# Kernel optimization log

Hardware: AMD Instinct MI355X
Metric: run time of the kernel (lower is better)

Reference implementation:

```python
import jax, jax.numpy as jnp
import numpy as np
from jax import lax

C = 256
HEADS = 8
H2 = HEADS // 2          # heads per branch
HD = C // HEADS          # head dim = 32
SR = 4                   # spatial reduction ratio
WS = 7                   # window size (hard-coded in source)
SCALE = HD ** -0.5
EPS = 1e-5


def _window_partition(t, H, W, D):
    # t: [B, h, N, c] -> [B*h*nW, WS^3, c]
    B, h, N, c = t.shape
    t = t.reshape(B * h, H // WS, WS, W // WS, WS, D // WS, WS, c)
    t = t.transpose(0, 1, 3, 5, 2, 4, 6, 7)
    return t.reshape(-1, WS * WS * WS, c)


def _window_reverse(w, H, W, D, head):
    # w: [BH*nW, WS^3, c] -> [B, N, head*c] (heads interleaved into channels)
    nW = (H // WS) * (W // WS) * (D // WS)
    BH = w.shape[0] // nW
    x = w.reshape(BH, H // WS, W // WS, D // WS, WS, WS, WS, -1)
    x = x.transpose(0, 1, 4, 2, 5, 3, 6, 7).reshape(BH, H, W, D, -1)
    B = BH // head
    x = x.reshape(B, head, H, W, D, -1).transpose(0, 2, 3, 4, 1, 5)
    return x.reshape(B, H * W * D, -1)


def setup_inputs() -> dict:
    key = jax.random.key(0)
    ks = jax.random.split(key, 16)
    B, H, W, D = 1, 28, 28, 28
    N = H * W * D
    tn = lambda k, shp: jax.random.normal(k, shp, jnp.float32) * 0.02
    # conv fan-out inits (per source _init_weights)
    lepe_fan = 3 * 3 * C // C  # depthwise: groups=C
    sr_fan = SR * SR * C
    return {
        "x": jax.random.normal(ks[0], (B, N, C), jnp.float32),
        "H": H, "W": W, "D": D,
        "lepe_w": tn(ks[1], (C, C)),
        "lepe_b": jnp.zeros((C,), jnp.float32),
        "lepe_conv_w": jax.random.normal(ks[2], (C, 1, 3, 3, 3), jnp.float32) * np.sqrt(2.0 / lepe_fan),
        "lepe_conv_b": jnp.zeros((C,), jnp.float32),
        "sr_w": jax.random.normal(ks[3], (C, C, SR, SR, SR), jnp.float32) * np.sqrt(2.0 / sr_fan),
        "sr_b": jnp.zeros((C,), jnp.float32),
        "norm_g": jnp.ones((C,), jnp.float32),
        "norm_b": jnp.zeros((C,), jnp.float32),
        "q1_w": tn(ks[4], (C // 2, C)),
        "kv1_w": tn(ks[5], (C, C)),
        "q2_w": tn(ks[6], (C // 2, C)),
        "kv2_w": tn(ks[7], (C, C)),
        "proj_w": tn(ks[8], (C, C)),
        "proj_b": jnp.zeros((C,), jnp.float32),
    }


def _forward(x, lepe_w, lepe_b, lepe_conv_w, lepe_conv_b, sr_w, sr_b,
             norm_g, norm_b, q1_w, kv1_w, q2_w, kv2_w, proj_w, proj_b,
             H, W, D):
    B, N, _ = x.shape
    # --- LePE: linear -> depthwise Conv3d over (H,W,D) ---
    y = x @ lepe_w.T + lepe_b                              # [B,N,C]
    y = y.transpose(0, 2, 1).reshape(B, C, H, W, D)
    lepe = lax.conv_general_dilated(
        y, lepe_conv_w, window_strides=(1, 1, 1), padding='SAME',
        dimension_numbers=('NCDHW', 'OIDHW', 'NCDHW'), feature_group_count=C)
    lepe = (lepe + lepe_conv_b[None, :, None, None, None])
    lepe = lepe.reshape(B, C, N).transpose(0, 2, 1)        # [B,N,C]

    x_ = x.transpose(0, 2, 1).reshape(B, C, H, W, D)

    # --- Branch 1: spatially-reduced global attention (heads 0..3) ---
    q1 = (x @ q1_w.T).reshape(B, N, H2, HD).transpose(0, 2, 1, 3)   # [B,h2,N,hd]
    x1 = lax.conv_general_dilated(
        x_, sr_w, window_strides=(SR, SR, SR), padding='VALID',
        dimension_numbers=('NCDHW', 'OIDHW', 'NCDHW'))
    x1 = x1 + sr_b[None, :, None, None, None]
    x1 = x1.reshape(B, C, -1).transpose(0, 2, 1)                    # [B,Nr,C]
    mu = x1.mean(-1, keepdims=True)
    var = ((x1 - mu) ** 2).mean(-1, keepdims=True)
    x1 = (x1 - mu) * lax.rsqrt(var + EPS) * norm_g + norm_b
    x1 = jax.nn.gelu(x1, approximate=False)
    Nr = x1.shape[1]
    kv1 = (x1 @ kv1_w.T).reshape(B, Nr, 2, H2, HD).transpose(2, 0, 3, 1, 4)
    k1, v1 = kv1[0], kv1[1]                                         # [B,h2,Nr,hd]
    attn1 = jax.nn.softmax(jnp.einsum('bhnd,bhmd->bhnm', q1, k1) * SCALE, axis=-1)
    o1 = jnp.einsum('bhnm,bhmd->bhnd', attn1, v1)
    o1 = o1.transpose(0, 2, 1, 3).reshape(B, N, C // 2)

    # --- Branch 2: windowed local attention (heads 4..7) ---
    q2 = (x @ q2_w.T).reshape(B, N, H2, HD).transpose(0, 2, 1, 3)
    kv2 = (x @ kv2_w.T).reshape(B, N, 2, H2, HD).transpose(2, 0, 3, 1, 4)
    k2, v2 = kv2[0], kv2[1]                                         # [B,h2,N,hd]
    q2w = _window_partition(q2, H, W, D)
    k2w = _window_partition(k2, H, W, D)
    v2w = _window_partition(v2, H, W, D)
    attn2 = jax.nn.softmax(jnp.einsum('wnd,wmd->wnm', q2w, k2w) * SCALE, axis=-1)
    o2 = jnp.einsum('wnm,wmd->wnd', attn2, v2w)
    o2 = _window_reverse(o2, H, W, D, H2)                           # [B,N,C/2]

    out = jnp.concatenate([o1, o2], axis=-1)
    return (out + lepe) @ proj_w.T + proj_b


def reference(x, H, W, D, lepe_w, lepe_b, lepe_conv_w, lepe_conv_b,
              sr_w, sr_b, norm_g, norm_b, q1_w, kv1_w, q2_w, kv2_w,
              proj_w, proj_b):
    return _forward(x, lepe_w, lepe_b, lepe_conv_w, lepe_conv_b, sr_w, sr_b,
                    norm_g, norm_b, q1_w, kv1_w, q2_w, kv2_w, proj_w, proj_b,
                    int(H), int(W), int(D))
```

## Files before the change

### kernel.cpp

```cpp
#include <hip/hip_runtime.h>

#define N_TOK 21952
#define NR    343
#define ATT_SCALE 0.17677669529663687f

typedef unsigned short u16;
typedef short  v8s __attribute__((ext_vector_type(8)));
typedef float  v4f __attribute__((ext_vector_type(4)));

__device__ __forceinline__ float bf2f(unsigned u) {
    return __builtin_bit_cast(float, u << 16);
}
__device__ __forceinline__ u16 f2bf(float f) {
    unsigned u = __builtin_bit_cast(unsigned, f);
    u += 0x7fffu + ((u >> 16) & 1u);
    return (u16)(u >> 16);
}
__device__ __forceinline__ unsigned bfadd2(unsigned a, unsigned b) {
    float lo = bf2f(a & 0xffffu) + bf2f(b & 0xffffu);
    float hi = bf2f(a >> 16)     + bf2f(b >> 16);
    return (unsigned)f2bf(lo) | ((unsigned)f2bf(hi) << 16);
}

__global__ __launch_bounds__(256) void convert_x_kernel(
    const float* __restrict__ x, u16* __restrict__ xb)
{
    size_t i = ((size_t)blockIdx.x * 256 + threadIdx.x) * 8;
    float4 a0 = *(const float4*)(x + i);
    float4 a1 = *(const float4*)(x + i + 4);
    uint4 av;
    av.x = (unsigned)f2bf(a0.x) | ((unsigned)f2bf(a0.y) << 16);
    av.y = (unsigned)f2bf(a0.z) | ((unsigned)f2bf(a0.w) << 16);
    av.z = (unsigned)f2bf(a1.x) | ((unsigned)f2bf(a1.y) << 16);
    av.w = (unsigned)f2bf(a1.z) | ((unsigned)f2bf(a1.w) << 16);
    *(uint4*)(xb + i) = av;
}

#define WSEG0 16384
#define WSEG1 24576
#define WSEG2 32768
#define WSEG3 49152
#define WSEG4 65536
#define WSEG5 81920
#define WSEG6 82112

__global__ __launch_bounds__(256) void convert_w_kernel(
    const float* __restrict__ wl,  const float* __restrict__ wq1,
    const float* __restrict__ wq2, const float* __restrict__ wk2,
    const float* __restrict__ wk1, const float* __restrict__ wp,
    const float* __restrict__ lepe_b,
    u16* wb_comb, u16* wb_k1, u16* wb_p, float* bias_all)
{
    int gid = blockIdx.x * 256 + threadIdx.x;
    if (gid >= WSEG6) return;
    if (gid >= WSEG5) {
        int b = gid - WSEG5;
        float4 v;
        int i = b * 4;
        v.x = (i + 0 < 256) ? lepe_b[i + 0] : 0.f;
        v.y = (i + 1 < 256) ? lepe_b[i + 1] : 0.f;
        v.z = (i + 2 < 256) ? lepe_b[i + 2] : 0.f;
        v.w = (i + 3 < 256) ? lepe_b[i + 3] : 0.f;
        *(float4*)(bias_all + i) = v;
        return;
    }
    const float* s; u16* d; int l; float sc = 1.f;
    if      (gid < WSEG0) { s = wl;  d = wb_comb;           l = gid; }
    else if (gid < WSEG1) { s = wq1; d = wb_comb + 65536;   l = gid - WSEG0; sc = ATT_SCALE; }
    else if (gid < WSEG2) { s = wq2; d = wb_comb + 98304;   l = gid - WSEG1; sc = ATT_SCALE; }
    else if (gid < WSEG3) { s = wk2; d = wb_comb + 131072;  l = gid - WSEG2; }
    else if (gid < WSEG4) { s = wk1; d = wb_k1;             l = gid - WSEG3; }
    else                  { s = wp;  d = wb_p;              l = gid - WSEG4; }
    float4 v = *(const float4*)(s + (size_t)l * 4);
    *(ushort4*)(d + (size_t)l * 4) =
        make_ushort4(f2bf(v.x * sc), f2bf(v.y * sc), f2bf(v.z * sc), f2bf(v.w * sc));
}

__global__ __launch_bounds__(256) void convert_sr_kernel(
    const float* __restrict__ wsr, u16* __restrict__ wt)
{
    int u  = blockIdx.x * 256 + threadIdx.x;
    int co = u >> 8, ci = u & 255;
    const float* src = wsr + (size_t)co * 16384 + ci * 64;
#pragma unroll
    for (int t4 = 0; t4 < 16; t4++) {
        float4 v = *(const float4*)(src + t4 * 4);
        int t = t4 * 4;
        wt[(size_t)(t + 0) * 65536 + co * 256 + ci] = f2bf(v.x);
        wt[(size_t)(t + 1) * 65536 + co * 256 + ci] = f2bf(v.y);
        wt[(size_t)(t + 2) * 65536 + co * 256 + ci] = f2bf(v.z);
        wt[(size_t)(t + 3) * 65536 + co * 256 + ci] = f2bf(v.w);
    }
}

#define LDA 40

__global__ __launch_bounds__(256) void gemm_bf16(
    const void* __restrict__ A, const u16* __restrict__ A2,
    const u16* __restrict__ W, const float* __restrict__ bias,
    void* __restrict__ outp, int M, int K, int ldout, int a_fp32, int mode)
{
    __shared__ u16 Asm[128 * LDA];
    __shared__ u16 Bsm[128 * LDA];
    const int tid = threadIdx.x;
    const int m0 = blockIdx.x * 128;
    const int n0 = blockIdx.y * 128;
    const int wave = tid >> 6, lane = tid & 63;
    const int wm = (wave & 1) * 64, wn = (wave >> 1) * 64;
    const int fr = lane & 15, fq = lane >> 4;

    v4f acc[4][4];
#pragma unroll
    for (int i = 0; i < 4; i++)
#pragma unroll
        for (int j = 0; j < 4; j++) acc[i][j] = (v4f){0.f, 0.f, 0.f, 0.f};

    for (int kk = 0; kk < K; kk += 32) {
#pragma unroll
        for (int i = 0; i < 2; i++) {
            int u = tid + i * 256;
            int r = u >> 2, kc = (u & 3) * 8;
            uint4 av = make_uint4(0, 0, 0, 0);
            int m = m0 + r;
            if (m < M) {
                if (a_fp32) {
                    const float* Af = (const float*)A + (size_t)m * K + kk + kc;
                    float4 a0 = *(const float4*)Af;
                    float4 a1 = *(const float4*)(Af + 4);
                    av.x = (unsigned)f2bf(a0.x) | ((unsigned)f2bf(a0.y) << 16);
                    av.y = (unsigned)f2bf(a0.z) | ((unsigned)f2bf(a0.w) << 16);
                    av.z = (unsigned)f2bf(a1.x) | ((unsigned)f2bf(a1.y) << 16);
                    av.w = (unsigned)f2bf(a1.z) | ((unsigned)f2bf(a1.w) << 16);
                } else {
                    av = *(const uint4*)((const u16*)A + (size_t)m * K + kk + kc);
                    if (A2) {
                        uint4 bv = *(const uint4*)(A2 + (size_t)m * K + kk + kc);
                        av.x = bfadd2(av.x, bv.x); av.y = bfadd2(av.y, bv.y);
                        av.z = bfadd2(av.z, bv.z); av.w = bfadd2(av.w, bv.w);
                    }
                }
            }
            *(uint4*)(Asm + r * LDA + kc) = av;
            uint4 wv = *(const uint4*)(W + (size_t)(n0 + r) * K + kk + kc);
            *(uint4*)(Bsm + r * LDA + kc) = wv;
        }
        __syncthreads();

        v8s af[4], bfr[4];
#pragma unroll
        for (int i = 0; i < 4; i++)
            af[i] = *(const v8s*)(Asm + (wm + i * 16 + fr) * LDA + fq * 8);
#pragma unroll
        for (int j = 0; j < 4; j++)
            bfr[j] = *(const v8s*)(Bsm + (wn + j * 16 + fr) * LDA + fq * 8);
#pragma unroll
        for (int i = 0; i < 4; i++)
#pragma unroll
            for (int j = 0; j < 4; j++)
                acc[i][j] = __builtin_amdgcn_mfma_f32_16x16x32_bf16(
                    af[i], bfr[j], acc[i][j], 0, 0, 0);
        __syncthreads();
    }

    float* outf = (float*)outp;
    u16*   outb = (u16*)outp;
#pragma unroll
    for (int i = 0; i < 4; i++) {
#pragma unroll
        for (int j = 0; j < 4; j++) {
            int col = n0 + wn + j * 16 + fr;
#pragma unroll
            for (int r = 0; r < 4; r++) {
                int row = m0 + wm + i * 16 + fq * 4 + r;
                if (row >= M) continue;
                float v = acc[i][j][r];
                if (bias) v += bias[col];
                if (mode == 0) outb[(size_t)row * ldout + col] = f2bf(v);
                else           outf[(size_t)row * ldout + col] = v;
            }
        }
    }
}

__global__ __launch_bounds__(256) void sr_gemm(
    const u16* __restrict__ xb, const u16* __restrict__ Wt,
    float* __restrict__ partials)
{
    __shared__ u16 Asm[128 * LDA];
    __shared__ u16 Bsm[128 * LDA];
    const int tid = threadIdx.x;
    const int m0 = blockIdx.x * 128;
    const int n0 = blockIdx.y * 128;
    const int z  = blockIdx.z;
    const int wave = tid >> 6, lane = tid & 63;
    const int wm = (wave & 1) * 64, wn = (wave >> 1) * 64;
    const int fr = lane & 15, fq = lane >> 4;

    v4f acc[4][4];
#pragma unroll
    for (int i = 0; i < 4; i++)
#pragma unroll
        for (int j = 0; j < 4; j++) acc[i][j] = (v4f){0.f, 0.f, 0.f, 0.f};

    for (int it = 0; it < 16; it++) {
        int tap = z * 2 + (it >> 3);
        int ci0 = (it & 7) * 32;
        int kz = tap >> 4, ky = (tap >> 2) & 3, kx = tap & 3;
#pragma unroll
        for (int i = 0; i < 2; i++) {
            int u = tid + i * 256;
            int r = u >> 2, seg = (u & 3) * 8;
            uint4 av = make_uint4(0, 0, 0, 0);
            int p = m0 + r;
            if (p < NR) {
                int pz = p / 49, pr = p % 49, py = pr / 7, px = pr % 7;
                int n = (pz * 4 + kz) * 784 + (py * 4 + ky) * 28 + (px * 4 + kx);
                av = *(const uint4*)(xb + (size_t)n * 256 + ci0 + seg);
            }
            *(uint4*)(Asm + r * LDA + seg) = av;
            uint4 wv = *(const uint4*)(Wt + (size_t)tap * 65536 +
                                       (size_t)(n0 + r) * 256 + ci0 + seg);
            *(uint4*)(Bsm + r * LDA + seg) = wv;
        }
        __syncthreads();

        v8s af[4], bfr[4];
#pragma unroll
        for (int i = 0; i < 4; i++)
            af[i] = *(const v8s*)(Asm + (wm + i * 16 + fr) * LDA + fq * 8);
#pragma unroll
        for (int j = 0; j < 4; j++)
            bfr[j] = *(const v8s*)(Bsm + (wn + j * 16 + fr) * LDA + fq * 8);
#pragma unroll
        for (int i = 0; i < 4; i++)
#pragma unroll
            for (int j = 0; j < 4; j++)
                acc[i][j] = __builtin_amdgcn_mfma_f32_16x16x32_bf16(
                    af[i], bfr[j], acc[i][j], 0, 0, 0);
        __syncthreads();
    }

    float* dst = partials + (size_t)z * (NR * 256);
#pragma unroll
    for (int i = 0; i < 4; i++) {
#pragma unroll
        for (int j = 0; j < 4; j++) {
            int col = n0 + wn + j * 16 + fr;
#pragma unroll
            for (int r = 0; r < 4; r++) {
                int row = m0 + wm + i * 16 + fq * 4 + r;
                if (row < NR) dst[(size_t)row * 256 + col] = acc[i][j][r];
            }
        }
    }
}

__global__ __launch_bounds__(256) void ln_gelu_kernel(
    const float* __restrict__ partials, const float* __restrict__ srb,
    const float* __restrict__ g, const float* __restrict__ b,
    u16* __restrict__ out)
{
    int row = blockIdx.x, c = threadIdx.x;
    float v = srb[c];
#pragma unroll
    for (int s = 0; s < 32; s++)
        v += partials[(size_t)s * (NR * 256) + row * 256 + c];
    float s1 = v, s2 = v * v;
#pragma unroll
    for (int off = 1; off < 64; off <<= 1) {
        s1 += __shfl_xor(s1, off);
        s2 += __shfl_xor(s2, off);
    }
    __shared__ float ws[4], ws2[4];
    int wave = c >> 6, lane = c & 63;
    if (lane == 0) { ws[wave] = s1; ws2[wave] = s2; }
    __syncthreads();
    float mean = (ws[0] + ws[1] + ws[2] + ws[3]) * (1.f / 256.f);
    float m2   = (ws2[0] + ws2[1] + ws2[2] + ws2[3]) * (1.f / 256.f);
    float var  = m2 - mean * mean;
    float xn = (v - mean) * rsqrtf(var + 1e-5f) * g[c] + b[c];
    out[row * 256 + c] = f2bf(0.5f * xn * (1.f + erff(xn * 0.70710678118654752f)));
}

__global__ __launch_bounds__(256) void dwconv_kernel(
    const u16* __restrict__ xall, const float* __restrict__ w,
    const float* __restrict__ bias, u16* __restrict__ out)
{
    __shared__ float sm[216 * 64];
    __shared__ float sw[64 * 27];
    const int tid = threadIdx.x;
    const int t  = blockIdx.x;
    const int g  = blockIdx.y;
    const int tz = t / 49, tr = t % 49, ty = tr / 7, tx = tr % 7;

    for (int u = tid; u < 64 * 27; u += 256) sw[u] = w[g * 64 * 27 + u];

    for (int u = tid; u < 216 * 8; u += 256) {
        int r = u >> 3, c8 = (u & 7) * 8;
        int vz = tz * 4 - 1 + r / 36;
        int rem = r % 36;
        int vy = ty * 4 - 1 + rem / 6;
        int vx = tx * 4 - 1 + rem % 6;
        float f[8];
        if ((unsigned)vz < 28u && (unsigned)vy < 28u && (unsigned)vx < 28u) {
            int n = vz * 784 + vy * 28 + vx;
            uint4 raw = *(const uint4*)(xall + (size_t)n * 768 + g * 64 + c8);
            f[0] = bf2f(raw.x & 0xffffu); f[1] = bf2f(raw.x >> 16);
            f[2] = bf2f(raw.y & 0xffffu); f[3] = bf2f(raw.y >> 16);
            f[4] = bf2f(raw.z & 0xffffu); f[5] = bf2f(raw.z >> 16);
            f[6] = bf2f(raw.w & 0xffffu); f[7] = bf2f(raw.w >> 16);
        } else {
#pragma unroll
            for (int i = 0; i < 8; i++) f[i] = 0.f;
        }
        float* dst = &sm[r * 64 + c8];
        *(float4*)dst       = make_float4(f[0], f[1], f[2], f[3]);
        *(float4*)(dst + 4) = make_float4(f[4], f[5], f[6], f[7]);
    }
    __syncthreads();

    const int c  = tid & 63;
    const int ch = g * 64 + c;
    float wreg[27];
#pragma unroll
    for (int j = 0; j < 27; j++) wreg[j] = sw[c * 27 + j];
    const float bc = bias[ch];

    const int vbase = (tid >> 6) * 16;
    for (int v = vbase; v < vbase + 16; v++) {
        int vz = v >> 4, vy = (v >> 2) & 3, vx = v & 3;
        float a = bc;
#pragma unroll
        for (int dz = 0; dz < 3; dz++)
#pragma unroll
            for (int dy = 0; dy < 3; dy++)
#pragma unroll
                for (int dx = 0; dx < 3; dx++)
                    a = fmaf(sm[((vz + dz) * 36 + (vy + dy) * 6 + (vx + dx)) * 64 + c],
                             wreg[dz * 9 + dy * 3 + dx], a);
        int n = (tz * 4 + vz) * 784 + (ty * 4 + vy) * 28 + (tx * 4 + vx);
        out[(size_t)n * 256 + ch] = f2bf(a);
    }
}

#define KP  40
#define VTP 360
#define PP  40

__global__ __launch_bounds__(256) void attn1_kernel(
    const u16* __restrict__ xall, const u16* __restrict__ kv1,
    u16* __restrict__ o)
{
    __shared__ u16 Ks[352 * KP];
    __shared__ u16 VTs[32 * VTP];
    __shared__ u16 Ps[4 * 16 * PP];
    const int tid = threadIdx.x;
    const int h = blockIdx.y;
    const int qbase = blockIdx.x * 352;
    const int mt0 = blockIdx.z * 11;
    const int wave = tid >> 6, lane = tid & 63;
    const int fr = lane & 15, fq = lane >> 4;

    for (int u = tid; u < 352 * 4; u += 256) {
        int r = u >> 2, seg = u & 3;
        uint4 kq = make_uint4(0, 0, 0, 0), vq = make_uint4(0, 0, 0, 0);
        if (r < NR) {
            kq = *(const uint4*)(kv1 + (size_t)r * 256 + h * 32 + seg * 8);
            vq = *(const uint4*)(kv1 + (size_t)r * 256 + 128 + h * 32 + seg * 8);
        }
        *(uint4*)(Ks + r * KP + seg * 8) = kq;
        int d0 = seg * 8;
        VTs[(d0 + 0) * VTP + r] = (u16)(vq.x & 0xffffu);
        VTs[(d0 + 1) * VTP + r] = (u16)(vq.x >> 16);
        VTs[(d0 + 2) * VTP + r] = (u16)(vq.y & 0xffffu);
        VTs[(d0 + 3) * VTP + r] = (u16)(vq.y >> 16);
        VTs[(d0 + 4) * VTP + r] = (u16)(vq.z & 0xffffu);
        VTs[(d0 + 5) * VTP + r] = (u16)(vq.z >> 16);
        VTs[(d0 + 6) * VTP + r] = (u16)(vq.w & 0xffffu);
        VTs[(d0 + 7) * VTP + r] = (u16)(vq.w >> 16);
    }
    __syncthreads();

    u16* Pw = Ps + wave * 16 * PP;
    for (int mt = mt0 + wave; mt < mt0 + 11; mt += 4) {
        int qrow = qbase + mt * 16 + fr;
        v8s aq = {0, 0, 0, 0, 0, 0, 0, 0};
        if (qrow < N_TOK)
            aq = *(const v8s*)(xall + (size_t)qrow * 768 + 256 + h * 32 + fq * 8);

        v4f s[22];
#pragma unroll
        for (int t = 0; t < 22; t++) {
            v8s bk = *(const v8s*)(Ks + (t * 16 + fr) * KP + fq * 8);
            s[t] = __builtin_amdgcn_mfma_f32_16x16x32_bf16(
                aq, bk, (v4f){0.f, 0.f, 0.f, 0.f}, 0, 0, 0);
        }
        if (fr >= 7) {
#pragma unroll
            for (int r = 0; r < 4; r++) s[21][r] = -1e30f;
        }

        float inv_l[4];
#pragma unroll
        for (int r = 0; r < 4; r++) {
            float m = s[0][r];
#pragma unroll
            for (int t = 1; t < 22; t++) m = fmaxf(m, s[t][r]);
#pragma unroll
            for (int off = 1; off < 16; off <<= 1) m = fmaxf(m, __shfl_xor(m, off));
            float l = 0.f;
#pragma unroll
            for (int t = 0; t < 22; t++) {
                v4f sv = s[t];
                float p = __expf(sv[r] - m);
                sv[r] = p; s[t] = sv;
                l += p;
            }
#pragma unroll
            for (int off = 1; off < 16; off <<= 1) l += __shfl_xor(l, off);
            inv_l[r] = 1.f / l;
        }

        v4f o0 = {0.f, 0.f, 0.f, 0.f}, o1 = {0.f, 0.f, 0.f, 0.f};
#pragma unroll
        for (int kt = 0; kt < 11; kt++) {
#pragma unroll
            for (int tt = 0; tt < 2; tt++) {
                int t = kt * 2 + tt;
#pragma unroll
                for (int r = 0; r < 4; r++)
                    Pw[(fq * 4 + r) * PP + tt * 16 + fr] = f2bf(s[t][r]);
            }
            __asm__ volatile("s_waitcnt lgkmcnt(0)" ::: "memory");
            v8s ap  = *(const v8s*)(Pw + fr * PP + fq * 8);
            v8s bv0 = *(const v8s*)(VTs + fr * VTP + kt * 32 + fq * 8);
            v8s bv1 = *(const v8s*)(VTs + (16 + fr) * VTP + kt * 32 + fq * 8);
            o0 = __builtin_amdgcn_mfma_f32_16x16x32_bf16(ap, bv0, o0, 0, 0, 0);
            o1 = __builtin_amdgcn_mfma_f32_16x16x32_bf16(ap, bv1, o1, 0, 0, 0);
        }

#pragma unroll
        for (int r = 0; r < 4; r++) {
            int n = qbase + mt * 16 + fq * 4 + r;
            if (n < N_TOK) {
                u16* op = o + (size_t)n * 256 + h * 32;
                op[fr]      = f2bf(o0[r] * inv_l[r]);
                op[16 + fr] = f2bf(o1[r] * inv_l[r]);
            }
        }
    }
}

__global__ __launch_bounds__(256) void attn2_kernel(
    const u16* __restrict__ xall, u16* __restrict__ o)
{
    __shared__ u16 Ks[352 * KP];
    __shared__ u16 VTs[32 * VTP];
    __shared__ u16 Ps[4 * 16 * PP];
    const int tid = threadIdx.x;
    const int h  = blockIdx.y;
    const int wi = blockIdx.x;
    const int zb = (wi >> 4) & 3, yb = (wi >> 2) & 3, xb = wi & 3;
    const int mt0 = blockIdx.z * 11;
    const int wave = tid >> 6, lane = tid & 63;
    const int fr = lane & 15, fq = lane >> 4;

    for (int u = tid; u < 352 * 4; u += 256) {
        int r = u >> 2, seg = u & 3;
        uint4 kq = make_uint4(0, 0, 0, 0), vq = make_uint4(0, 0, 0, 0);
        if (r < NR) {
            int mz = r / 49, mr = r % 49, my = mr / 7, mx = mr % 7;
            int nk = (zb * 7 + mz) * 784 + (yb * 7 + my) * 28 + (xb * 7 + mx);
            const u16* base = xall + (size_t)nk * 768 + 512;
            kq = *(const uint4*)(base + h * 32 + seg * 8);
            vq = *(const uint4*)(base + 128 + h * 32 + seg * 8);
        }
        *(uint4*)(Ks + r * KP + seg * 8) = kq;
        int d0 = seg * 8;
        VTs[(d0 + 0) * VTP + r] = (u16)(vq.x & 0xffffu);
        VTs[(d0 + 1) * VTP + r] = (u16)(vq.x >> 16);
        VTs[(d0 + 2) * VTP + r] = (u16)(vq.y & 0xffffu);
        VTs[(d0 + 3) * VTP + r] = (u16)(vq.y >> 16);
        VTs[(d0 + 4) * VTP + r] = (u16)(vq.z & 0xffffu);
        VTs[(d0 + 5) * VTP + r] = (u16)(vq.z >> 16);
        VTs[(d0 + 6) * VTP + r] = (u16)(vq.w & 0xffffu);
        VTs[(d0 + 7) * VTP + r] = (u16)(vq.w >> 16);
    }
    __syncthreads();

    u16* Pw = Ps + wave * 16 * PP;
    for (int mt = mt0 + wave; mt < mt0 + 11; mt += 4) {
        int tw = mt * 16 + fr;
        v8s aq = {0, 0, 0, 0, 0, 0, 0, 0};
        if (tw < NR) {
            int wz = tw / 49, tr2 = tw % 49, wy = tr2 / 7, wx = tr2 % 7;
            int nq = (zb * 7 + wz) * 784 + (yb * 7 + wy) * 28 + (xb * 7 + wx);
            aq = *(const v8s*)(xall + (size_t)nq * 768 + 384 + h * 32 + fq * 8);
        }

        v4f s[22];
#pragma unroll
        for (int t = 0; t < 22; t++) {
            v8s bk = *(const v8s*)(Ks + (t * 16 + fr) * KP + fq * 8);
            s[t] = __builtin_amdgcn_mfma_f32_16x16x32_bf16(
                aq, bk, (v4f){0.f, 0.f, 0.f, 0.f}, 0, 0, 0);
        }
        if (fr >= 7) {
#pragma unroll
            for (int r = 0; r < 4; r++) s[21][r] = -1e30f;
        }

        float inv_l[4];
#pragma unroll
        for (int r = 0; r < 4; r++) {
            float m = s[0][r];
#pragma unroll
            for (int t = 1; t < 22; t++) m = fmaxf(m, s[t][r]);
#pragma unroll
            for (int off = 1; off < 16; off <<= 1) m = fmaxf(m, __shfl_xor(m, off));
            float l = 0.f;
#pragma unroll
            for (int t = 0; t < 22; t++) {
                v4f sv = s[t];
                float p = __expf(sv[r] - m);
                sv[r] = p; s[t] = sv;
                l += p;
            }
#pragma unroll
            for (int off = 1; off < 16; off <<= 1) l += __shfl_xor(l, off);
            inv_l[r] = 1.f / l;
        }

        v4f o0 = {0.f, 0.f, 0.f, 0.f}, o1 = {0.f, 0.f, 0.f, 0.f};
#pragma unroll
        for (int kt = 0; kt < 11; kt++) {
#pragma unroll
            for (int tt = 0; tt < 2; tt++) {
                int t = kt * 2 + tt;
#pragma unroll
                for (int r = 0; r < 4; r++)
                    Pw[(fq * 4 + r) * PP + tt * 16 + fr] = f2bf(s[t][r]);
            }
            __asm__ volatile("s_waitcnt lgkmcnt(0)" ::: "memory");
            v8s ap  = *(const v8s*)(Pw + fr * PP + fq * 8);
            v8s bv0 = *(const v8s*)(VTs + fr * VTP + kt * 32 + fq * 8);
            v8s bv1 = *(const v8s*)(VTs + (16 + fr) * VTP + kt * 32 + fq * 8);
            o0 = __builtin_amdgcn_mfma_f32_16x16x32_bf16(ap, bv0, o0, 0, 0, 0);
            o1 = __builtin_amdgcn_mfma_f32_16x16x32_bf16(ap, bv1, o1, 0, 0, 0);
        }

#pragma unroll
        for (int r = 0; r < 4; r++) {
            int ts = mt * 16 + fq * 4 + r;
            if (ts < NR) {
                int wz = ts / 49, tr2 = ts % 49, wy = tr2 / 7, wx = tr2 % 7;
                int nq = (zb * 7 + wz) * 784 + (yb * 7 + wy) * 28 + (xb * 7 + wx);
                u16* op = o + (size_t)nq * 256 + 128 + h * 32;
                op[fr]      = f2bf(o0[r] * inv_l[r]);
                op[16 + fr] = f2bf(o1[r] * inv_l[r]);
            }
        }
    }
}

extern "C" void kernel_launch(void* const* d_in, const int* in_sizes, int n_in,
                              void* d_out, int out_size, void* d_ws, size_t ws_size,
                              hipStream_t stream)
{
    const float* x       = (const float*)d_in[0];
    const float* lepe_w  = (const float*)d_in[4];
    const float* lepe_b  = (const float*)d_in[5];
    const float* lconv_w = (const float*)d_in[6];
    const float* lconv_b = (const float*)d_in[7];
    const float* sr_w    = (const float*)d_in[8];
    const float* sr_b    = (const float*)d_in[9];
    const float* norm_g  = (const float*)d_in[10];
    const float* norm_b  = (const float*)d_in[11];
    const float* q1_w    = (const float*)d_in[12];
    const float* kv1_w   = (const float*)d_in[13];
    const float* q2_w    = (const float*)d_in[14];
    const float* kv2_w   = (const float*)d_in[15];
    const float* proj_w  = (const float*)d_in[16];
    const float* proj_b  = (const float*)d_in[17];
    float* out = (float*)d_out;

    const size_t NC = (size_t)N_TOK * 256;

    float* partials = (float*)d_ws;
    float* bias_all = partials + 32 * (NR * 256);
    u16* xb     = (u16*)(bias_all + 768);
    u16* xall   = xb + NC;
    u16* lepeb  = xall + (size_t)N_TOK * 768;
    u16* colb   = lepeb + NC;
    u16* x1b    = colb + NC;
    u16* kv1b   = x1b + NR * 256;
    u16* wb_comb = kv1b + NR * 256;
    u16* wb_k1  = wb_comb + 196608;
    u16* wb_p   = wb_k1 + 65536;
    u16* wsr_t  = wb_p + 65536;
    size_t need = (size_t)(32 * NR * 256 + 768) * 4 +
                  (NC + (size_t)N_TOK * 768 + 3 * NC + 2 * (size_t)NR * 256 +
                   196608 + 2 * 65536 + 4194304) * 2;
    if (ws_size < need) return;

    convert_w_kernel<<<dim3(321), 256, 0, stream>>>(
        lepe_w, q1_w, q2_w, kv2_w, kv1_w, proj_w, lepe_b,
        wb_comb, wb_k1, wb_p, bias_all);
    convert_sr_kernel<<<dim3(256), 256, 0, stream>>>(sr_w, wsr_t);
    convert_x_kernel<<<dim3(2744), 256, 0, stream>>>(x, xb);
    gemm_bf16<<<dim3(172, 6), 256, 0, stream>>>(xb, nullptr, wb_comb, bias_all,
                                                xall, N_TOK, 256, 768, 0, 0);
    dwconv_kernel<<<dim3(343, 4), 256, 0, stream>>>(xall, lconv_w, lconv_b, lepeb);
    sr_gemm<<<dim3(3, 2, 32), 256, 0, stream>>>(xb, wsr_t, partials);
    ln_gelu_kernel<<<dim3(NR), 256, 0, stream>>>(partials, sr_b, norm_g, norm_b, x1b);
    gemm_bf16<<<dim3(3, 2), 256, 0, stream>>>(x1b, nullptr, wb_k1, nullptr,
                                              kv1b, NR, 256, 256, 0, 0);
    attn1_kernel<<<dim3(63, 4, 2), 256, 0, stream>>>(xall, kv1b, colb);
    attn2_kernel<<<dim3(64, 4, 2), 256, 0, stream>>>(xall, colb);
    gemm_bf16<<<dim3(172, 2), 256, 0, stream>>>(colb, lepeb, wb_p, proj_b,
                                                out, N_TOK, 256, 256, 0, 1);
}
```

Before: 293.4 us.

## Rewrite GEMMs as one-shot full-K 64x64 tiles with XOR-swizzled LDS

Replaces the K-looped 128x128 GEMM, which used a padded LDS tile and a barrier pair per K step, with a kernel that loads the whole K=256 slab of A and W into XOR-swizzled shared memory at once and then runs 8 MFMA steps without further barriers. Tiles shrink to 64x64, giving many more blocks, and the bf16 output is staged through LDS so global stores are coalesced 16-byte writes. The SR conv GEMM gets the same treatment, loading each tap's full channel range in one go. The cost is 64 KB of LDS per block, which limits occupancy, plus more redundant reloads of A and W from the smaller tiles.

```diff
diff --git a/kernel.cpp b/kernel.cpp
--- a/kernel.cpp
+++ b/kernel.cpp
@@ -21,6 +21,8 @@
     float hi = bf2f(a >> 16)     + bf2f(b >> 16);
     return (unsigned)f2bf(lo) | ((unsigned)f2bf(hi) << 16);
 }
+
+#define SWZ(r, g) ((((g) ^ ((r) & 7))) * 8)
 
 __global__ __launch_bounds__(256) void convert_x_kernel(
     const float* __restrict__ x, u16* __restrict__ xb)
@@ -93,158 +95,199 @@
     }
 }
 
-#define LDA 40
-
-__global__ __launch_bounds__(256) void gemm_bf16(
-    const void* __restrict__ A, const u16* __restrict__ A2,
+__global__ __launch_bounds__(256) void gemm_os(
+    const u16* __restrict__ A, const u16* __restrict__ A2,
     const u16* __restrict__ W, const float* __restrict__ bias,
-    void* __restrict__ outp, int M, int K, int ldout, int a_fp32, int mode)
-{
-    __shared__ u16 Asm[128 * LDA];
-    __shared__ u16 Bsm[128 * LDA];
+    void* __restrict__ outp, int M, int ldout, int mode)
+{
+    __shared__ u16 Asm[64 * 256];
+    __shared__ u16 Bsm[64 * 256];
     const int tid = threadIdx.x;
-    const int m0 = blockIdx.x * 128;
-    const int n0 = blockIdx.y * 128;
+    const int n0 = blockIdx.x * 64;
+    const int m0 = blockIdx.y * 64;
     const int wave = tid >> 6, lane = tid & 63;
-    const int wm = (wave & 1) * 64, wn = (wave >> 1) * 64;
+    const int wm = (wave & 1) * 32, wn = (wave >> 1) * 32;
     const int fr = lane & 15, fq = lane >> 4;
 
-    v4f acc[4][4];
-#pragma unroll
-    for (int i = 0; i < 4; i++)
-#pragma unroll
-        for (int j = 0; j < 4; j++) acc[i][j] = (v4f){0.f, 0.f, 0.f, 0.f};
-
-    for (int kk = 0; kk < K; kk += 32) {
+    uint4 pa[8], pb[8], pa2[8];
+#pragma unroll
+    for (int i = 0; i < 8; i++) {
+        int u = i * 256 + tid;
+        int r = u >> 5, seg = (u & 31) * 8;
+        int m = m0 + r;
+        uint4 av = make_uint4(0, 0, 0, 0);
+        if (m < M) av = *(const uint4*)(A + (size_t)m * 256 + seg);
+        pa[i] = av;
+        if (A2) {
+            uint4 bv = make_uint4(0, 0, 0, 0);
+            if (m < M) bv = *(const uint4*)(A2 + (size_t)m * 256 + seg);
+            pa2[i] = bv;
+        }
+        pb[i] = *(const uint4*)(W + (size_t)(n0 + r) * 256 + seg);
+    }
+#pragma unroll
+    for (int i = 0; i < 8; i++) {
+        int u = i * 256 + tid;
+        int r = u >> 5, g = u & 31;
+        uint4 av = pa[i];
+        if (A2) {
+            av.x = bfadd2(av.x, pa2[i].x); av.y = bfadd2(av.y, pa2[i].y);
+            av.z = bfadd2(av.z, pa2[i].z); av.w = bfadd2(av.w, pa2[i].w);
+        }
+        *(uint4*)(Asm + r * 256 + SWZ(r, g)) = av;
+        *(uint4*)(Bsm + r * 256 + SWZ(r, g)) = pb[i];
+    }
+    __syncthreads();
+
+    v4f acc[2][2];
+#pragma unroll
+    for (int i = 0; i < 2; i++)
+#pragma unroll
+        for (int j = 0; j < 2; j++) acc[i][j] = (v4f){0.f, 0.f, 0.f, 0.f};
+
+#pragma unroll
+    for (int ks = 0; ks < 8; ks++) {
+        v8s af[2], bfj[2];
 #pragma unroll
         for (int i = 0; i < 2; i++) {
-            int u = tid + i * 256;
-            int r = u >> 2, kc = (u & 3) * 8;
-            uint4 av = make_uint4(0, 0, 0, 0);
-            int m = m0 + r;
-            if (m < M) {
-                if (a_fp32) {
-                    const float* Af = (const float*)A + (size_t)m * K + kk + kc;
-                    float4 a0 = *(const float4*)Af;
-                    float4 a1 = *(const float4*)(Af + 4);
-                    av.x = (unsigned)f2bf(a0.x) | ((unsigned)f2bf(a0.y) << 16);
-                    av.y = (unsigned)f2bf(a0.z) | ((unsigned)f2bf(a0.w) << 16);
-                    av.z = (unsigned)f2bf(a1.x) | ((unsigned)f2bf(a1.y) << 16);
-                    av.w = (unsigned)f2bf(a1.z) | ((unsigned)f2bf(a1.w) << 16);
-                } else {
-                    av = *(const uint4*)((const u16*)A + (size_t)m * K + kk + kc);
-                    if (A2) {
-                        uint4 bv = *(const uint4*)(A2 + (size_t)m * K + kk + kc);
-                        av.x = bfadd2(av.x, bv.x); av.y = bfadd2(av.y, bv.y);
-                        av.z = bfadd2(av.z, bv.z); av.w = bfadd2(av.w, bv.w);
-                    }
+            int row = wm + i * 16 + fr;
+            af[i] = *(const v8s*)(Asm + row * 256 + SWZ(row, ks * 4 + fq));
+        }
+#pragma unroll
+        for (int j = 0; j < 2; j++) {
+            int row = wn + j * 16 + fr;
+            bfj[j] = *(const v8s*)(Bsm + row * 256 + SWZ(row, ks * 4 + fq));
+        }
+#pragma unroll
+        for (int i = 0; i < 2; i++)
+#pragma unroll
+            for (int j = 0; j < 2; j++)
+                acc[i][j] = __builtin_amdgcn_mfma_f32_16x16x32_bf16(
+                    af[i], bfj[j], acc[i][j], 0, 0, 0);
+    }
+
+    if (mode == 1) {
+        float* outf = (float*)outp;
+#pragma unroll
+        for (int i = 0; i < 2; i++)
+#pragma unroll
+            for (int j = 0; j < 2; j++) {
+                int col = n0 + wn + j * 16 + fr;
+                float bv = bias ? bias[col] : 0.f;
+#pragma unroll
+                for (int r = 0; r < 4; r++) {
+                    int row = m0 + wm + i * 16 + fq * 4 + r;
+                    if (row < M)
+                        outf[(size_t)row * ldout + col] = acc[i][j][r] + bv;
                 }
             }
-            *(uint4*)(Asm + r * LDA + kc) = av;
-            uint4 wv = *(const uint4*)(W + (size_t)(n0 + r) * K + kk + kc);
-            *(uint4*)(Bsm + r * LDA + kc) = wv;
-        }
-        __syncthreads();
-
-        v8s af[4], bfr[4];
-#pragma unroll
-        for (int i = 0; i < 4; i++)
-            af[i] = *(const v8s*)(Asm + (wm + i * 16 + fr) * LDA + fq * 8);
-#pragma unroll
-        for (int j = 0; j < 4; j++)
-            bfr[j] = *(const v8s*)(Bsm + (wn + j * 16 + fr) * LDA + fq * 8);
-#pragma unroll
-        for (int i = 0; i < 4; i++)
-#pragma unroll
-            for (int j = 0; j < 4; j++)
-                acc[i][j] = __builtin_amdgcn_mfma_f32_16x16x32_bf16(
-                    af[i], bfr[j], acc[i][j], 0, 0, 0);
-        __syncthreads();
-    }
-
-    float* outf = (float*)outp;
-    u16*   outb = (u16*)outp;
-#pragma unroll
-    for (int i = 0; i < 4; i++) {
-#pragma unroll
-        for (int j = 0; j < 4; j++) {
-            int col = n0 + wn + j * 16 + fr;
+        return;
+    }
+    __syncthreads();
+    u16* ot = Asm;
+#pragma unroll
+    for (int i = 0; i < 2; i++)
+#pragma unroll
+        for (int j = 0; j < 2; j++) {
+            int col = wn + j * 16 + fr;
+            float bv = bias ? bias[n0 + col] : 0.f;
 #pragma unroll
             for (int r = 0; r < 4; r++) {
-                int row = m0 + wm + i * 16 + fq * 4 + r;
-                if (row >= M) continue;
-                float v = acc[i][j][r];
-                if (bias) v += bias[col];
-                if (mode == 0) outb[(size_t)row * ldout + col] = f2bf(v);
-                else           outf[(size_t)row * ldout + col] = v;
-            }
-        }
-    }
-}
-
-__global__ __launch_bounds__(256) void sr_gemm(
+                int row = wm + i * 16 + fq * 4 + r;
+                ot[row * 72 + col] = f2bf(acc[i][j][r] + bv);
+            }
+        }
+    __syncthreads();
+    u16* outb = (u16*)outp;
+#pragma unroll
+    for (int k2 = 0; k2 < 2; k2++) {
+        int u = k2 * 256 + tid;
+        int r = u >> 3, cs = (u & 7) * 8;
+        int row = m0 + r;
+        if (row < M)
+            *(uint4*)(outb + (size_t)row * ldout + n0 + cs) =
+                *(const uint4*)(ot + r * 72 + cs);
+    }
+}
+
+__global__ __launch_bounds__(256) void sr_gemm_os(
     const u16* __restrict__ xb, const u16* __restrict__ Wt,
     float* __restrict__ partials)
 {
-    __shared__ u16 Asm[128 * LDA];
-    __shared__ u16 Bsm[128 * LDA];
+    __shared__ u16 Asm[64 * 256];
+    __shared__ u16 Bsm[64 * 256];
     const int tid = threadIdx.x;
-    const int m0 = blockIdx.x * 128;
-    const int n0 = blockIdx.y * 128;
+    const int n0 = blockIdx.x * 64;
+    const int m0 = blockIdx.y * 64;
     const int z  = blockIdx.z;
     const int wave = tid >> 6, lane = tid & 63;
-    const int wm = (wave & 1) * 64, wn = (wave >> 1) * 64;
+    const int wm = (wave & 1) * 32, wn = (wave >> 1) * 32;
     const int fr = lane & 15, fq = lane >> 4;
 
-    v4f acc[4][4];
-#pragma unroll
-    for (int i = 0; i < 4; i++)
-#pragma unroll
-        for (int j = 0; j < 4; j++) acc[i][j] = (v4f){0.f, 0.f, 0.f, 0.f};
-
-    for (int it = 0; it < 16; it++) {
-        int tap = z * 2 + (it >> 3);
-        int ci0 = (it & 7) * 32;
+    v4f acc[2][2];
+#pragma unroll
+    for (int i = 0; i < 2; i++)
+#pragma unroll
+        for (int j = 0; j < 2; j++) acc[i][j] = (v4f){0.f, 0.f, 0.f, 0.f};
+
+    for (int t = 0; t < 2; t++) {
+        int tap = z * 2 + t;
         int kz = tap >> 4, ky = (tap >> 2) & 3, kx = tap & 3;
-#pragma unroll
-        for (int i = 0; i < 2; i++) {
-            int u = tid + i * 256;
-            int r = u >> 2, seg = (u & 3) * 8;
+        int koff = kz * 784 + ky * 28 + kx;
+
+        uint4 pa[8], pb[8];
+#pragma unroll
+        for (int i = 0; i < 8; i++) {
+            int u = i * 256 + tid;
+            int r = u >> 5, seg = (u & 31) * 8;
+            int p = m0 + r;
             uint4 av = make_uint4(0, 0, 0, 0);
-            int p = m0 + r;
             if (p < NR) {
                 int pz = p / 49, pr = p % 49, py = pr / 7, px = pr % 7;
-                int n = (pz * 4 + kz) * 784 + (py * 4 + ky) * 28 + (px * 4 + kx);
-                av = *(const uint4*)(xb + (size_t)n * 256 + ci0 + seg);
-            }
-            *(uint4*)(Asm + r * LDA + seg) = av;
-            uint4 wv = *(const uint4*)(Wt + (size_t)tap * 65536 +
-                                       (size_t)(n0 + r) * 256 + ci0 + seg);
-            *(uint4*)(Bsm + r * LDA + seg) = wv;
+                int n = pz * 4 * 784 + py * 4 * 28 + px * 4 + koff;
+                av = *(const uint4*)(xb + (size_t)n * 256 + seg);
+            }
+            pa[i] = av;
+            pb[i] = *(const uint4*)(Wt + (size_t)tap * 65536 +
+                                    (size_t)(n0 + r) * 256 + seg);
+        }
+        if (t == 1) __syncthreads();
+#pragma unroll
+        for (int i = 0; i < 8; i++) {
+            int u = i * 256 + tid;
+            int r = u >> 5, g = u & 31;
+            *(uint4*)(Asm + r * 256 + SWZ(r, g)) = pa[i];
+            *(uint4*)(Bsm + r * 256 + SWZ(r, g)) = pb[i];
         }
         __syncthreads();
 
-        v8s af[4], bfr[4];
-#pragma unroll
-        for (int i = 0; i < 4; i++)
-            af[i] = *(const v8s*)(Asm + (wm + i * 16 + fr) * LDA + fq * 8);
-#pragma unroll
-        for (int j = 0; j < 4; j++)
-            bfr[j] = *(const v8s*)(Bsm + (wn + j * 16 + fr) * LDA + fq * 8);
-#pragma unroll
-        for (int i = 0; i < 4; i++)
-#pragma unroll
-            for (int j = 0; j < 4; j++)
-                acc[i][j] = __builtin_amdgcn_mfma_f32_16x16x32_bf16(
-                    af[i], bfr[j], acc[i][j], 0, 0, 0);
-        __syncthreads();
+#pragma unroll
+        for (int ks = 0; ks < 8; ks++) {
+            v8s af[2], bfj[2];
+#pragma unroll
+            for (int i = 0; i < 2; i++) {
+                int row = wm + i * 16 + fr;
+                af[i] = *(const v8s*)(Asm + row * 256 + SWZ(row, ks * 4 + fq));
+            }
+#pragma unroll
+            for (int j = 0; j < 2; j++) {
+                int row = wn + j * 16 + fr;
+                bfj[j] = *(const v8s*)(Bsm + row * 256 + SWZ(row, ks * 4 + fq));
+            }
+#pragma unroll
+            for (int i = 0; i < 2; i++)
+#pragma unroll
+                for (int j = 0; j < 2; j++)
+                    acc[i][j] = __builtin_amdgcn_mfma_f32_16x16x32_bf16(
+                        af[i], bfj[j], acc[i][j], 0, 0, 0);
+        }
     }
 
     float* dst = partials + (size_t)z * (NR * 256);
 #pragma unroll
-    for (int i = 0; i < 4; i++) {
-#pragma unroll
-        for (int j = 0; j < 4; j++) {
+    for (int i = 0; i < 2; i++)
+#pragma unroll
+        for (int j = 0; j < 2; j++) {
             int col = n0 + wn + j * 16 + fr;
 #pragma unroll
             for (int r = 0; r < 4; r++) {
@@ -252,7 +295,6 @@
                 if (row < NR) dst[(size_t)row * 256 + col] = acc[i][j][r];
             }
         }
-    }
 }
 
 __global__ __launch_bounds__(256) void ln_gelu_kernel(
@@ -608,15 +650,15 @@
         wb_comb, wb_k1, wb_p, bias_all);
     convert_sr_kernel<<<dim3(256), 256, 0, stream>>>(sr_w, wsr_t);
     convert_x_kernel<<<dim3(2744), 256, 0, stream>>>(x, xb);
-    gemm_bf16<<<dim3(172, 6), 256, 0, stream>>>(xb, nullptr, wb_comb, bias_all,
-                                                xall, N_TOK, 256, 768, 0, 0);
+    gemm_os<<<dim3(12, 343), 256, 0, stream>>>(xb, nullptr, wb_comb, bias_all,
+                                               xall, N_TOK, 768, 0);
     dwconv_kernel<<<dim3(343, 4), 256, 0, stream>>>(xall, lconv_w, lconv_b, lepeb);
-    sr_gemm<<<dim3(3, 2, 32), 256, 0, stream>>>(xb, wsr_t, partials);
+    sr_gemm_os<<<dim3(4, 6, 32), 256, 0, stream>>>(xb, wsr_t, partials);
     ln_gelu_kernel<<<dim3(NR), 256, 0, stream>>>(partials, sr_b, norm_g, norm_b, x1b);
-    gemm_bf16<<<dim3(3, 2), 256, 0, stream>>>(x1b, nullptr, wb_k1, nullptr,
-                                              kv1b, NR, 256, 256, 0, 0);
+    gemm_os<<<dim3(4, 6), 256, 0, stream>>>(x1b, nullptr, wb_k1, nullptr,
+                                            kv1b, NR, 256, 0);
     attn1_kernel<<<dim3(63, 4, 2), 256, 0, stream>>>(xall, kv1b, colb);
     attn2_kernel<<<dim3(64, 4, 2), 256, 0, stream>>>(xall, colb);
-    gemm_bf16<<<dim3(172, 2), 256, 0, stream>>>(colb, lepeb, wb_p, proj_b,
-                                                out, N_TOK, 256, 256, 0, 1);
-}
+    gemm_os<<<dim3(4, 343), 256, 0, stream>>>(colb, lepeb, wb_p, proj_b,
+                                              out, N_TOK, 256, 1);
+}
```

New measurement: 306.3 us. +4.4%, slower.
